# Kernel tuning notes

Hardware: AMD Instinct MI355X
Metric: run time of the kernel (lower is better)

The kernel has to match this reference:

```python
import jax, jax.numpy as jnp
import numpy as np

B, SQ, SK = 32, 512, 512
Q_DIM = 512
K_DIM = 512
H = 8
HD = 64
INNER = H * HD
MAX_POS = 512
SCALE = 1.0 / np.sqrt(HD)


def setup_inputs() -> dict:
    key = jax.random.key(0)
    ks = jax.random.split(key, 10)
    query = jax.random.normal(ks[0], (B, SQ, Q_DIM), dtype=jnp.float32)
    key_t = jax.random.normal(ks[1], (B, SK, K_DIM), dtype=jnp.float32)
    value = jax.random.normal(ks[2], (B, SK, K_DIM), dtype=jnp.float32)
    mask = jax.random.randint(ks[3], (B, SQ, SK), 0, 2, dtype=jnp.int32)
    # learned parameters (Linear weights stored as [in, out]; to_q/k/v have no bias)
    Wq = jax.random.normal(ks[4], (Q_DIM, INNER), dtype=jnp.float32) * 0.02
    Wk = jax.random.normal(ks[5], (K_DIM, INNER), dtype=jnp.float32) * 0.02
    Wv = jax.random.normal(ks[6], (K_DIM, INNER), dtype=jnp.float32) * 0.02
    Wo = jax.random.normal(ks[7], (INNER, Q_DIM), dtype=jnp.float32) * 0.02
    bo = jnp.zeros((Q_DIM,), dtype=jnp.float32)
    rel_pos_emb = jax.random.normal(ks[8], (MAX_POS, MAX_POS), dtype=jnp.float32) * 0.02
    return {"query": query, "key": key_t, "value": value, "mask": mask,
            "Wq": Wq, "Wk": Wk, "Wv": Wv, "Wo": Wo, "bo": bo,
            "rel_pos_emb": rel_pos_emb}


def reference(query, key, value, mask, Wq, Wk, Wv, Wo, bo, rel_pos_emb):
    # Projections (no bias for q/k/v)
    q = query @ Wq   # [B, SQ, INNER]
    k = key @ Wk     # [B, SK, INNER]
    v = value @ Wv   # [B, SK, INNER]
    # split heads -> [B, H, S, HD]
    q = q.reshape(B, SQ, H, HD).transpose(0, 2, 1, 3)
    k = k.reshape(B, SK, H, HD).transpose(0, 2, 1, 3)
    v = v.reshape(B, SK, H, HD).transpose(0, 2, 1, 3)
    # scaled scores + learned relative-position bias (shared across batch/heads)
    scores = jnp.einsum('bhqd,bhkd->bhqk', q, k) * SCALE
    bias = rel_pos_emb[:SQ, :SK]          # [SQ, SK]
    scores = scores + bias[None, None, :, :]
    # additive masking: positions where mask == 0 get -inf
    scores = jnp.where(mask[:, None, :, :] == 0, -jnp.inf, scores)
    attn = jax.nn.softmax(scores, axis=-1)
    # dropout is identity in eval mode (p treated as inference)
    out = jnp.einsum('bhqk,bhkd->bhqd', attn, v)
    out = out.transpose(0, 2, 1, 3).reshape(B, SQ, INNER)
    return out @ Wo + bo
```

## Files before the change

kernel.cpp:

```cpp
#include <hip/hip_runtime.h>
#include <stdint.h>


typedef unsigned short u16;
typedef __attribute__((ext_vector_type(4))) float f32x4;
typedef __attribute__((ext_vector_type(8))) __bf16 bf16x8;
typedef __attribute__((ext_vector_type(4))) unsigned short u16x4;
typedef __attribute__((ext_vector_type(8))) unsigned short u16x8;
typedef __attribute__((ext_vector_type(4))) int i32x4;
typedef __attribute__((ext_vector_type(4))) _Float16 f16x4;
typedef __attribute__((ext_vector_type(8))) _Float16 f16x8;

#define MFMA16(a, b, c) __builtin_amdgcn_mfma_f32_16x16x32_bf16((a), (b), (c), 0, 0, 0)

__device__ __forceinline__ u16 f2bf(float f) {
  unsigned u = __float_as_uint(f);
  u += 0x7fffu + ((u >> 16) & 1u);
  return (u16)(u >> 16);
}
__device__ __forceinline__ float bf2f(u16 h) {
  return __uint_as_float(((unsigned)h) << 16);
}

__device__ __forceinline__ void gl_lds16(const void* g, void* l) {
  __builtin_amdgcn_global_load_lds(
      (const __attribute__((address_space(1))) unsigned int*)g,
      (__attribute__((address_space(3))) unsigned int*)l, 16, 0, 0);
}

__global__ __launch_bounds__(256) void k_prep(
    const float* __restrict__ Wq, const float* __restrict__ Wk,
    const float* __restrict__ Wv, const float* __restrict__ Wo,
    u16* __restrict__ Wt, u16* __restrict__ WoHi, u16* __restrict__ WoLo) {
  int idx = blockIdx.x * 256 + threadIdx.x;
  int n = idx >> 9, k = idx & 511;
  int src = k * 512 + n;
  Wt[idx]          = f2bf(Wq[src]);
  Wt[262144 + idx] = f2bf(Wk[src]);
  Wt[524288 + idx] = f2bf(Wv[src]);
  float wo = Wo[src];
  u16 hi = f2bf(wo);
  WoHi[idx] = hi;
  WoLo[idx] = f2bf(wo - bf2f(hi));
}

__global__ __launch_bounds__(256) void k_mb(
    const int* __restrict__ mask, const float* __restrict__ bias,
    _Float16* __restrict__ MB) {
  size_t i8 = ((size_t)blockIdx.x * 256 + threadIdx.x) * 8;
  i32x4 m0 = *(const i32x4*)&mask[i8];
  i32x4 m1 = *(const i32x4*)&mask[i8 + 4];
  size_t bi = i8 & 262143;
  f32x4 b0 = *(const f32x4*)&bias[bi];
  f32x4 b1 = *(const f32x4*)&bias[bi + 4];
  const _Float16 MASKED = (_Float16)(-60000.0f);
  f16x8 o;
#pragma unroll
  for (int e = 0; e < 4; ++e) {
    o[e]     = (m0[e] != 0) ? (_Float16)b0[e] : MASKED;
    o[e + 4] = (m1[e] != 0) ? (_Float16)b1[e] : MASKED;
  }
  *(f16x8*)&MB[i8] = o;
}

__global__ __launch_bounds__(512) void k_proj(
    const float* __restrict__ Xq, const float* __restrict__ Xk, const float* __restrict__ Xv,
    const u16* __restrict__ Wt,
    u16* __restrict__ Qb, u16* __restrict__ Kb, u16* __restrict__ Vtb) {
  __shared__ u16 lA[128][40];
  __shared__ u16 lB[256][40];
  const int mat = blockIdx.z;
  const float* __restrict__ A = (mat == 0) ? Xq : (mat == 1) ? Xk : Xv;
  const u16* __restrict__ Bw = Wt + (size_t)mat * 262144;
  const int tid = threadIdx.x;
  const int lane = tid & 63, wid = tid >> 6;
  const int wm = wid >> 2, wn = wid & 3;
  const int m0 = blockIdx.y * 128, n0 = blockIdx.x * 256;
  const int fr = lane & 15, g = lane >> 4;
  const int arow = tid >> 3, acg = tid & 7;
  f32x4 acc[4][4] = {};

  for (int kt = 0; kt < 16; ++kt) {
    const int k0 = kt * 32;
#pragma unroll
    for (int p = 0; p < 2; ++p) {
      int row = p * 64 + arow;
      f32x4 v = *(const f32x4*)&A[(size_t)(m0 + row) * 512 + k0 + acg * 4];
      u16x4 hv;
      hv[0] = f2bf(v[0]); hv[1] = f2bf(v[1]); hv[2] = f2bf(v[2]); hv[3] = f2bf(v[3]);
      *(u16x4*)&lA[row][acg * 4] = hv;
    }
#pragma unroll
    for (int p = 0; p < 2; ++p) {
      int idx = p * 512 + tid;
      int row = idx >> 2, cg = idx & 3;
      *(u16x8*)&lB[row][cg * 8] = *(const u16x8*)&Bw[(size_t)(n0 + row) * 512 + k0 + cg * 8];
    }
    __syncthreads();
    bf16x8 af[4], bfr[4];
#pragma unroll
    for (int fm = 0; fm < 4; ++fm)
      af[fm] = *(const bf16x8*)&lA[wm * 64 + fm * 16 + fr][g * 8];
#pragma unroll
    for (int fn = 0; fn < 4; ++fn)
      bfr[fn] = *(const bf16x8*)&lB[wn * 64 + fn * 16 + fr][g * 8];
#pragma unroll
    for (int fm = 0; fm < 4; ++fm)
#pragma unroll
      for (int fn = 0; fn < 4; ++fn)
        acc[fm][fn] = MFMA16(af[fm], bfr[fn], acc[fm][fn]);
    __syncthreads();
  }

  if (mat < 2) {
    u16* __restrict__ Out = (mat == 0) ? Qb : Kb;
#pragma unroll
    for (int fm = 0; fm < 4; ++fm) {
#pragma unroll
      for (int fn = 0; fn < 4; ++fn) {
        int gn = n0 + wn * 64 + fn * 16 + fr;
        int hh = gn >> 6, hd = gn & 63;
#pragma unroll
        for (int r = 0; r < 4; ++r) {
          int gm = m0 + wm * 64 + fm * 16 + g * 4 + r;
          int b = gm >> 9, sq = gm & 511;
          Out[(size_t)((b * 8 + hh) * 512 + sq) * 64 + hd] = f2bf(acc[fm][fn][r]);
        }
      }
    }
  } else {
#pragma unroll
    for (int fm = 0; fm < 4; ++fm) {
      int gm0 = m0 + wm * 64 + fm * 16 + g * 4;
      int b = gm0 >> 9, sq0 = gm0 & 511;
#pragma unroll
      for (int fn = 0; fn < 4; ++fn) {
        int gn = n0 + wn * 64 + fn * 16 + fr;
        int hh = gn >> 6, hd = gn & 63;
        u16x4 pv;
        pv[0] = f2bf(acc[fm][fn][0]); pv[1] = f2bf(acc[fm][fn][1]);
        pv[2] = f2bf(acc[fm][fn][2]); pv[3] = f2bf(acc[fm][fn][3]);
        *(u16x4*)&Vtb[(size_t)((b * 8 + hh) * 64 + hd) * 512 + sq0] = pv;
      }
    }
  }
}

__global__ __launch_bounds__(256, 4) void k_attn(
    const u16* __restrict__ Qb, const u16* __restrict__ Kb, const u16* __restrict__ Vtb,
    const _Float16* __restrict__ MB, float* __restrict__ Obuf) {
  __shared__ __align__(16) u16 kbuf[2][64][64];
  __shared__ __align__(16) u16 vbuf[2][64][64];
  __shared__ __align__(16) u16 lP[4][16][64];
  const int tid = threadIdx.x, lane = tid & 63, w = tid >> 6;
  const int orig = blockIdx.x;
  const int xcd = orig & 7, idx = orig >> 3;
  const int qq = idx & 3, h = (idx >> 2) & 7;
  const int b = xcd + 8 * (idx >> 5);
  const int bh = b * 8 + h;
  const int fr = lane & 15, g = lane >> 4;
  const int sq0 = qq * 128 + w * 32;
  const int sw = (fr & 7) << 4;
  const u16* __restrict__ Qh = Qb + (size_t)bh * 32768;
  const u16* __restrict__ Kh = Kb + (size_t)bh * 32768;
  const u16* __restrict__ Vh = Vtb + (size_t)bh * 32768;
  const _Float16* __restrict__ MBr = MB + (size_t)b * 262144 + (size_t)(sq0 + fr) * 512;
  char* lProw = (char*)&lP[w][fr][0];
  const char* kcb;
  const char* vcb;

  const int sub = lane >> 3;
  const int xo = ((lane & 7) ^ sub) * 8;

  bf16x8 qf[2][2];
#pragma unroll
  for (int qfi = 0; qfi < 2; ++qfi)
#pragma unroll
    for (int kc = 0; kc < 2; ++kc)
      qf[qfi][kc] = *(const bf16x8*)&Qh[(size_t)(sq0 + qfi * 16 + fr) * 64 + kc * 32 + g * 8];

  f32x4 oacc[2][4] = {};
  float mrow[2] = {-1e30f, -1e30f}, lrow[2] = {0.f, 0.f};

  {
    if (w < 2) {
      const int rb = w * 32;
      const u16* gs = Kh + (size_t)(rb + sub) * 64 + xo;
#pragma unroll
      for (int i = 0; i < 4; ++i)
        gl_lds16(gs + (size_t)i * 8 * 64, &kbuf[0][rb + i * 8][0]);
    } else {
      const int rb = (w - 2) * 32;
      const u16* gs = Vh + (size_t)(rb + sub) * 512 + xo;
#pragma unroll
      for (int i = 0; i < 4; ++i)
        gl_lds16(gs + (size_t)i * 8 * 512, &vbuf[0][rb + i * 8][0]);
    }
  }
  __syncthreads();

  int cur = 0;
  for (int kt = 0; kt < 8; ++kt) {
    const int sk0 = kt * 64;
    f16x4 mbv[2][4];
#pragma unroll
    for (int qfi = 0; qfi < 2; ++qfi)
#pragma unroll
      for (int fn = 0; fn < 4; ++fn)
        mbv[qfi][fn] = *(const f16x4*)&MBr[(size_t)qfi * 16 * 512 + sk0 + fn * 16 + g * 4];
    if (kt < 7) {
      const int nb = cur ^ 1, sk0n = sk0 + 64;
      if (w < 2) {
        const int rb = w * 32;
        const u16* gs = Kh + (size_t)(sk0n + rb + sub) * 64 + xo;
#pragma unroll
        for (int i = 0; i < 4; ++i)
          gl_lds16(gs + (size_t)i * 8 * 64, &kbuf[nb][rb + i * 8][0]);
      } else {
        const int rb = (w - 2) * 32;
        const u16* gs = Vh + (size_t)(rb + sub) * 512 + sk0n + xo;
#pragma unroll
        for (int i = 0; i < 4; ++i)
          gl_lds16(gs + (size_t)i * 8 * 512, &vbuf[nb][rb + i * 8][0]);
      }
    }
    kcb = (const char*)kbuf[cur];
    vcb = (const char*)vbuf[cur];
    f32x4 sacc[2][4] = {};
#pragma unroll
    for (int fn = 0; fn < 4; ++fn) {
      const int r = fn * 16 + fr;
      bf16x8 kf0 = *(const bf16x8*)(kcb + (size_t)r * 128 + ((0 * 64 + g * 16) ^ sw));
      bf16x8 kf1 = *(const bf16x8*)(kcb + (size_t)r * 128 + ((1 * 64 + g * 16) ^ sw));
      sacc[0][fn] = MFMA16(kf0, qf[0][0], sacc[0][fn]);
      sacc[0][fn] = MFMA16(kf1, qf[0][1], sacc[0][fn]);
      sacc[1][fn] = MFMA16(kf0, qf[1][0], sacc[1][fn]);
      sacc[1][fn] = MFMA16(kf1, qf[1][1], sacc[1][fn]);
    }
#pragma unroll
    for (int qfi = 0; qfi < 2; ++qfi)
#pragma unroll
      for (int fn = 0; fn < 4; ++fn)
#pragma unroll
        for (int r = 0; r < 4; ++r)
          sacc[qfi][fn][r] = sacc[qfi][fn][r] * 0.125f + (float)mbv[qfi][fn][r];

#pragma unroll
    for (int qfi = 0; qfi < 2; ++qfi) {
      float t0 = fmaxf(fmaxf(sacc[qfi][0][0], sacc[qfi][0][1]),
                       fmaxf(sacc[qfi][0][2], sacc[qfi][0][3]));
      float t1 = fmaxf(fmaxf(sacc[qfi][1][0], sacc[qfi][1][1]),
                       fmaxf(sacc[qfi][1][2], sacc[qfi][1][3]));
      float t2 = fmaxf(fmaxf(sacc[qfi][2][0], sacc[qfi][2][1]),
                       fmaxf(sacc[qfi][2][2], sacc[qfi][2][3]));
      float t3 = fmaxf(fmaxf(sacc[qfi][3][0], sacc[qfi][3][1]),
                       fmaxf(sacc[qfi][3][2], sacc[qfi][3][3]));
      float pm = fmaxf(fmaxf(t0, t1), fmaxf(t2, t3));
      pm = fmaxf(pm, __shfl_xor(pm, 16));
      pm = fmaxf(pm, __shfl_xor(pm, 32));
      if (!__all(pm - mrow[qfi] <= 8.0f)) {
        float mn = fmaxf(mrow[qfi], pm);
        float sfac = __expf(mrow[qfi] - mn);
        mrow[qfi] = mn;
        lrow[qfi] *= sfac;
#pragma unroll
        for (int r = 0; r < 4; ++r) {
          float sr = __shfl(sfac, g * 4 + r);
#pragma unroll
          for (int fnh = 0; fnh < 4; ++fnh)
            oacc[qfi][fnh][r] *= sr;
        }
      }
      float ps = 0.f;
#pragma unroll
      for (int fn = 0; fn < 4; ++fn) {
        float p0 = __expf(sacc[qfi][fn][0] - mrow[qfi]);
        float p1 = __expf(sacc[qfi][fn][1] - mrow[qfi]);
        float p2 = __expf(sacc[qfi][fn][2] - mrow[qfi]);
        float p3 = __expf(sacc[qfi][fn][3] - mrow[qfi]);
        ps += (p0 + p1) + (p2 + p3);
        u16x4 pw;
        pw[0] = f2bf(p0); pw[1] = f2bf(p1); pw[2] = f2bf(p2); pw[3] = f2bf(p3);
        *(u16x4*)(lProw + ((fn * 32 + g * 8) ^ sw)) = pw;
      }
      ps += __shfl_xor(ps, 16);
      ps += __shfl_xor(ps, 32);
      lrow[qfi] += ps;
      __builtin_amdgcn_wave_barrier();
#pragma unroll
      for (int kc = 0; kc < 2; ++kc) {
        bf16x8 pf = *(const bf16x8*)(lProw + ((kc * 64 + g * 16) ^ sw));
#pragma unroll
        for (int fnh = 0; fnh < 4; ++fnh) {
          const int vr = fnh * 16 + fr;
          bf16x8 vf = *(const bf16x8*)(vcb + (size_t)vr * 128 + ((kc * 64 + g * 16) ^ sw));
          oacc[qfi][fnh] = MFMA16(pf, vf, oacc[qfi][fnh]);
        }
      }
      __builtin_amdgcn_wave_barrier();
    }
    __syncthreads();
    cur ^= 1;
  }
#pragma unroll
  for (int qfi = 0; qfi < 2; ++qfi) {
#pragma unroll
    for (int r = 0; r < 4; ++r) {
      float lr = __shfl(lrow[qfi], g * 4 + r);
      float inv = 1.0f / lr;
      const int sq = sq0 + qfi * 16 + g * 4 + r;
      float* orow = &Obuf[((size_t)b * 512 + sq) * 512 + h * 64];
#pragma unroll
      for (int fnh = 0; fnh < 4; ++fnh)
        orow[fnh * 16 + fr] = oacc[qfi][fnh][r] * inv;
    }
  }
}

__global__ __launch_bounds__(512) void k_out(
    const float* __restrict__ Oin, const u16* __restrict__ WoHi, const u16* __restrict__ WoLo,
    const float* __restrict__ bo, float* __restrict__ out) {
  __shared__ u16 lAh[128][40], lAl[128][40];
  __shared__ u16 lBh[256][40], lBl[256][40];
  const int tid = threadIdx.x;
  const int lane = tid & 63, wid = tid >> 6;
  const int wm = wid >> 2, wn = wid & 3;
  const int m0 = blockIdx.y * 128, n0 = blockIdx.x * 256;
  const int fr = lane & 15, g = lane >> 4;
  const int arow = tid >> 3, acg = tid & 7;
  f32x4 acc[4][4] = {};

  for (int kt = 0; kt < 16; ++kt) {
    const int k0 = kt * 32;
#pragma unroll
    for (int p = 0; p < 2; ++p) {
      int row = p * 64 + arow;
      f32x4 v = *(const f32x4*)&Oin[(size_t)(m0 + row) * 512 + k0 + acg * 4];
      u16x4 hv, lv;
#pragma unroll
      for (int e = 0; e < 4; ++e) {
        u16 hb = f2bf(v[e]);
        hv[e] = hb;
        lv[e] = f2bf(v[e] - bf2f(hb));
      }
      *(u16x4*)&lAh[row][acg * 4] = hv;
      *(u16x4*)&lAl[row][acg * 4] = lv;
    }
#pragma unroll
    for (int p = 0; p < 2; ++p) {
      int idx = p * 512 + tid;
      int row = idx >> 2, cg = idx & 3;
      *(u16x8*)&lBh[row][cg * 8] = *(const u16x8*)&WoHi[(size_t)(n0 + row) * 512 + k0 + cg * 8];
      *(u16x8*)&lBl[row][cg * 8] = *(const u16x8*)&WoLo[(size_t)(n0 + row) * 512 + k0 + cg * 8];
    }
    __syncthreads();
    bf16x8 ah[4], al[4];
#pragma unroll
    for (int fm = 0; fm < 4; ++fm) {
      ah[fm] = *(const bf16x8*)&lAh[wm * 64 + fm * 16 + fr][g * 8];
      al[fm] = *(const bf16x8*)&lAl[wm * 64 + fm * 16 + fr][g * 8];
    }
#pragma unroll
    for (int fn = 0; fn < 4; ++fn) {
      bf16x8 bh = *(const bf16x8*)&lBh[wn * 64 + fn * 16 + fr][g * 8];
      bf16x8 bl = *(const bf16x8*)&lBl[wn * 64 + fn * 16 + fr][g * 8];
#pragma unroll
      for (int fm = 0; fm < 4; ++fm) {
        acc[fm][fn] = MFMA16(ah[fm], bh, acc[fm][fn]);
        acc[fm][fn] = MFMA16(ah[fm], bl, acc[fm][fn]);
        acc[fm][fn] = MFMA16(al[fm], bh, acc[fm][fn]);
      }
    }
    __syncthreads();
  }
#pragma unroll
  for (int fm = 0; fm < 4; ++fm) {
#pragma unroll
    for (int fn = 0; fn < 4; ++fn) {
      int gn = n0 + wn * 64 + fn * 16 + fr;
      float bv = bo[gn];
#pragma unroll
      for (int r = 0; r < 4; ++r) {
        int gm = m0 + wm * 64 + fm * 16 + g * 4 + r;
        out[(size_t)gm * 512 + gn] = acc[fm][fn][r] + bv;
      }
    }
  }
}

extern "C" void kernel_launch(void* const* d_in, const int* in_sizes, int n_in,
                              void* d_out, int out_size, void* d_ws, size_t ws_size,
                              hipStream_t stream) {
  (void)in_sizes; (void)n_in; (void)out_size; (void)ws_size;
  const float* query = (const float*)d_in[0];
  const float* key_t = (const float*)d_in[1];
  const float* value = (const float*)d_in[2];
  const int*   mask  = (const int*)d_in[3];
  const float* Wq    = (const float*)d_in[4];
  const float* Wk    = (const float*)d_in[5];
  const float* Wv    = (const float*)d_in[6];
  const float* Wo    = (const float*)d_in[7];
  const float* bo    = (const float*)d_in[8];
  const float* bias  = (const float*)d_in[9];
  float* out = (float*)d_out;

  char* p = (char*)d_ws;
  u16* Wt   = (u16*)p; p += (size_t)3 * 512 * 512 * 2;
  u16* WoHi = (u16*)p; p += (size_t)512 * 512 * 2;
  u16* WoLo = (u16*)p; p += (size_t)512 * 512 * 2;
  u16* Qb   = (u16*)p; p += (size_t)32 * 8 * 512 * 64 * 2;
  u16* Kb   = (u16*)p; p += (size_t)32 * 8 * 512 * 64 * 2;
  u16* Vtb  = (u16*)p; p += (size_t)32 * 8 * 512 * 64 * 2;
  float* Obuf = (float*)p; p += (size_t)32 * 512 * 512 * 4;
  _Float16* MBp = (_Float16*)p;

  k_prep<<<1024, 256, 0, stream>>>(Wq, Wk, Wv, Wo, Wt, WoHi, WoLo);
  k_mb<<<4096, 256, 0, stream>>>(mask, bias, MBp);
  k_proj<<<dim3(2, 128, 3), 512, 0, stream>>>(query, key_t, value, Wt, Qb, Kb, Vtb);
  k_attn<<<1024, 256, 0, stream>>>(Qb, Kb, Vtb, MBp, Obuf);
  k_out<<<dim3(2, 128), 512, 0, stream>>>(Obuf, WoHi, WoLo, bo, out);
}
```

Measured before the change: 185.4 us.

## Restructure projection and output GEMMs with direct-register weight loads and double-buffered A tiles

```diff
diff --git a/kernel.cpp b/kernel.cpp
--- a/kernel.cpp
+++ b/kernel.cpp
@@ -12,6 +12,13 @@
 typedef __attribute__((ext_vector_type(8))) _Float16 f16x8;
 
 #define MFMA16(a, b, c) __builtin_amdgcn_mfma_f32_16x16x32_bf16((a), (b), (c), 0, 0, 0)
+
+#define LGKM0_BARRIER()                                        \
+  do {                                                         \
+    asm volatile("s_waitcnt lgkmcnt(0)" ::: "memory");         \
+    __builtin_amdgcn_s_barrier();                              \
+    __builtin_amdgcn_sched_barrier(0);                         \
+  } while (0)
 
 __device__ __forceinline__ u16 f2bf(float f) {
   unsigned u = __float_as_uint(f);
@@ -63,53 +70,68 @@
   *(f16x8*)&MB[i8] = o;
 }
 
-__global__ __launch_bounds__(512) void k_proj(
+__global__ __launch_bounds__(256, 4) void k_proj(
     const float* __restrict__ Xq, const float* __restrict__ Xk, const float* __restrict__ Xv,
     const u16* __restrict__ Wt,
     u16* __restrict__ Qb, u16* __restrict__ Kb, u16* __restrict__ Vtb) {
-  __shared__ u16 lA[128][40];
-  __shared__ u16 lB[256][40];
+  __shared__ __align__(16) u16 lA[2][64][40];
   const int mat = blockIdx.z;
   const float* __restrict__ A = (mat == 0) ? Xq : (mat == 1) ? Xk : Xv;
   const u16* __restrict__ Bw = Wt + (size_t)mat * 262144;
-  const int tid = threadIdx.x;
-  const int lane = tid & 63, wid = tid >> 6;
-  const int wm = wid >> 2, wn = wid & 3;
-  const int m0 = blockIdx.y * 128, n0 = blockIdx.x * 256;
+  const int tid = threadIdx.x, lane = tid & 63, wn = tid >> 6;
+  const int m0 = blockIdx.y * 64, n0 = blockIdx.x * 256;
   const int fr = lane & 15, g = lane >> 4;
-  const int arow = tid >> 3, acg = tid & 7;
+  const int arow = tid >> 2, acg = tid & 3;
+  const float* __restrict__ Ar = &A[(size_t)(m0 + arow) * 512 + acg * 8];
+  const u16* __restrict__ Bp[4];
+#pragma unroll
+  for (int fn = 0; fn < 4; ++fn)
+    Bp[fn] = &Bw[(size_t)(n0 + wn * 64 + fn * 16 + fr) * 512 + g * 8];
+
   f32x4 acc[4][4] = {};
-
+  f32x4 va[2][2];
+  bf16x8 bB[4];
+
+  {
+    f32x4 v0 = *(const f32x4*)&Ar[0];
+    f32x4 v1 = *(const f32x4*)&Ar[4];
+    va[0][0] = *(const f32x4*)&Ar[32];
+    va[0][1] = *(const f32x4*)&Ar[36];
+    u16x8 hv;
+#pragma unroll
+    for (int e = 0; e < 4; ++e) { hv[e] = f2bf(v0[e]); hv[e + 4] = f2bf(v1[e]); }
+    *(u16x8*)&lA[0][arow][acg * 8] = hv;
+  }
+  LGKM0_BARRIER();
+
+#pragma unroll
   for (int kt = 0; kt < 16; ++kt) {
+    const int cur = kt & 1, nxt = cur ^ 1;
     const int k0 = kt * 32;
 #pragma unroll
-    for (int p = 0; p < 2; ++p) {
-      int row = p * 64 + arow;
-      f32x4 v = *(const f32x4*)&A[(size_t)(m0 + row) * 512 + k0 + acg * 4];
-      u16x4 hv;
-      hv[0] = f2bf(v[0]); hv[1] = f2bf(v[1]); hv[2] = f2bf(v[2]); hv[3] = f2bf(v[3]);
-      *(u16x4*)&lA[row][acg * 4] = hv;
-    }
-#pragma unroll
-    for (int p = 0; p < 2; ++p) {
-      int idx = p * 512 + tid;
-      int row = idx >> 2, cg = idx & 3;
-      *(u16x8*)&lB[row][cg * 8] = *(const u16x8*)&Bw[(size_t)(n0 + row) * 512 + k0 + cg * 8];
-    }
-    __syncthreads();
-    bf16x8 af[4], bfr[4];
-#pragma unroll
-    for (int fm = 0; fm < 4; ++fm)
-      af[fm] = *(const bf16x8*)&lA[wm * 64 + fm * 16 + fr][g * 8];
-#pragma unroll
     for (int fn = 0; fn < 4; ++fn)
-      bfr[fn] = *(const bf16x8*)&lB[wn * 64 + fn * 16 + fr][g * 8];
-#pragma unroll
-    for (int fm = 0; fm < 4; ++fm)
+      bB[fn] = *(const bf16x8*)(Bp[fn] + k0);
+    if (kt < 14) {
+      va[nxt][0] = *(const f32x4*)&Ar[(kt + 2) * 32];
+      va[nxt][1] = *(const f32x4*)&Ar[(kt + 2) * 32 + 4];
+    }
+#pragma unroll
+    for (int fm = 0; fm < 4; ++fm) {
+      bf16x8 af = *(const bf16x8*)&lA[cur][fm * 16 + fr][g * 8];
 #pragma unroll
       for (int fn = 0; fn < 4; ++fn)
-        acc[fm][fn] = MFMA16(af[fm], bfr[fn], acc[fm][fn]);
-    __syncthreads();
+        acc[fm][fn] = MFMA16(af, bB[fn], acc[fm][fn]);
+    }
+    if (kt < 15) {
+      u16x8 hv;
+#pragma unroll
+      for (int e = 0; e < 4; ++e) {
+        hv[e]     = f2bf(va[cur][0][e]);
+        hv[e + 4] = f2bf(va[cur][1][e]);
+      }
+      *(u16x8*)&lA[nxt][arow][acg * 8] = hv;
+    }
+    LGKM0_BARRIER();
   }
 
   if (mat < 2) {
@@ -122,7 +144,7 @@
         int hh = gn >> 6, hd = gn & 63;
 #pragma unroll
         for (int r = 0; r < 4; ++r) {
-          int gm = m0 + wm * 64 + fm * 16 + g * 4 + r;
+          int gm = m0 + fm * 16 + g * 4 + r;
           int b = gm >> 9, sq = gm & 511;
           Out[(size_t)((b * 8 + hh) * 512 + sq) * 64 + hd] = f2bf(acc[fm][fn][r]);
         }
@@ -131,7 +153,7 @@
   } else {
 #pragma unroll
     for (int fm = 0; fm < 4; ++fm) {
-      int gm0 = m0 + wm * 64 + fm * 16 + g * 4;
+      int gm0 = m0 + fm * 16 + g * 4;
       int b = gm0 >> 9, sq0 = gm0 & 511;
 #pragma unroll
       for (int fn = 0; fn < 4; ++fn) {
@@ -317,71 +339,88 @@
   }
 }
 
-__global__ __launch_bounds__(512) void k_out(
+__global__ __launch_bounds__(512, 4) void k_out(
     const float* __restrict__ Oin, const u16* __restrict__ WoHi, const u16* __restrict__ WoLo,
     const float* __restrict__ bo, float* __restrict__ out) {
-  __shared__ u16 lAh[128][40], lAl[128][40];
-  __shared__ u16 lBh[256][40], lBl[256][40];
-  const int tid = threadIdx.x;
-  const int lane = tid & 63, wid = tid >> 6;
-  const int wm = wid >> 2, wn = wid & 3;
-  const int m0 = blockIdx.y * 128, n0 = blockIdx.x * 256;
+  __shared__ __align__(16) u16 lAh[2][64][40], lAl[2][64][40];
+  const int tid = threadIdx.x, lane = tid & 63, wn = tid >> 6;
+  const int m0 = blockIdx.y * 64, n0 = blockIdx.x * 256;
   const int fr = lane & 15, g = lane >> 4;
   const int arow = tid >> 3, acg = tid & 7;
-  f32x4 acc[4][4] = {};
-
+  const float* __restrict__ Ar = &Oin[(size_t)(m0 + arow) * 512 + acg * 4];
+  const u16* __restrict__ Bh[2];
+  const u16* __restrict__ Bl[2];
+#pragma unroll
+  for (int fn = 0; fn < 2; ++fn) {
+    size_t row = (size_t)(n0 + wn * 32 + fn * 16 + fr) * 512 + g * 8;
+    Bh[fn] = &WoHi[row];
+    Bl[fn] = &WoLo[row];
+  }
+
+  f32x4 acc[4][2] = {};
+  f32x4 va[2];
+
+  {
+    f32x4 v = *(const f32x4*)&Ar[0];
+    va[0] = *(const f32x4*)&Ar[32];
+    u16x4 hv, lv;
+#pragma unroll
+    for (int e = 0; e < 4; ++e) {
+      u16 hb = f2bf(v[e]);
+      hv[e] = hb;
+      lv[e] = f2bf(v[e] - bf2f(hb));
+    }
+    *(u16x4*)&lAh[0][arow][acg * 4] = hv;
+    *(u16x4*)&lAl[0][arow][acg * 4] = lv;
+  }
+  LGKM0_BARRIER();
+
+#pragma unroll
   for (int kt = 0; kt < 16; ++kt) {
+    const int cur = kt & 1, nxt = cur ^ 1;
     const int k0 = kt * 32;
-#pragma unroll
-    for (int p = 0; p < 2; ++p) {
-      int row = p * 64 + arow;
-      f32x4 v = *(const f32x4*)&Oin[(size_t)(m0 + row) * 512 + k0 + acg * 4];
+    bf16x8 bh[2], bl[2];
+#pragma unroll
+    for (int fn = 0; fn < 2; ++fn) {
+      bh[fn] = *(const bf16x8*)(Bh[fn] + k0);
+      bl[fn] = *(const bf16x8*)(Bl[fn] + k0);
+    }
+    if (kt < 14)
+      va[nxt] = *(const f32x4*)&Ar[(kt + 2) * 32];
+#pragma unroll
+    for (int fm = 0; fm < 4; ++fm) {
+      bf16x8 ah = *(const bf16x8*)&lAh[cur][fm * 16 + fr][g * 8];
+      bf16x8 al = *(const bf16x8*)&lAl[cur][fm * 16 + fr][g * 8];
+#pragma unroll
+      for (int fn = 0; fn < 2; ++fn) {
+        acc[fm][fn] = MFMA16(ah, bh[fn], acc[fm][fn]);
+        acc[fm][fn] = MFMA16(ah, bl[fn], acc[fm][fn]);
+        acc[fm][fn] = MFMA16(al, bh[fn], acc[fm][fn]);
+      }
+    }
+    if (kt < 15) {
       u16x4 hv, lv;
 #pragma unroll
       for (int e = 0; e < 4; ++e) {
-        u16 hb = f2bf(v[e]);
+        u16 hb = f2bf(va[cur][e]);
         hv[e] = hb;
-        lv[e] = f2bf(v[e] - bf2f(hb));
-      }
-      *(u16x4*)&lAh[row][acg * 4] = hv;
-      *(u16x4*)&lAl[row][acg * 4] = lv;
-    }
-#pragma unroll
-    for (int p = 0; p < 2; ++p) {
-      int idx = p * 512 + tid;
-      int row = idx >> 2, cg = idx & 3;
-      *(u16x8*)&lBh[row][cg * 8] = *(const u16x8*)&WoHi[(size_t)(n0 + row) * 512 + k0 + cg * 8];
-      *(u16x8*)&lBl[row][cg * 8] = *(const u16x8*)&WoLo[(size_t)(n0 + row) * 512 + k0 + cg * 8];
-    }
-    __syncthreads();
-    bf16x8 ah[4], al[4];
-#pragma unroll
-    for (int fm = 0; fm < 4; ++fm) {
-      ah[fm] = *(const bf16x8*)&lAh[wm * 64 + fm * 16 + fr][g * 8];
-      al[fm] = *(const bf16x8*)&lAl[wm * 64 + fm * 16 + fr][g * 8];
-    }
-#pragma unroll
-    for (int fn = 0; fn < 4; ++fn) {
-      bf16x8 bh = *(const bf16x8*)&lBh[wn * 64 + fn * 16 + fr][g * 8];
-      bf16x8 bl = *(const bf16x8*)&lBl[wn * 64 + fn * 16 + fr][g * 8];
-#pragma unroll
-      for (int fm = 0; fm < 4; ++fm) {
-        acc[fm][fn] = MFMA16(ah[fm], bh, acc[fm][fn]);
-        acc[fm][fn] = MFMA16(ah[fm], bl, acc[fm][fn]);
-        acc[fm][fn] = MFMA16(al[fm], bh, acc[fm][fn]);
-      }
-    }
-    __syncthreads();
-  }
+        lv[e] = f2bf(va[cur][e] - bf2f(hb));
+      }
+      *(u16x4*)&lAh[nxt][arow][acg * 4] = hv;
+      *(u16x4*)&lAl[nxt][arow][acg * 4] = lv;
+    }
+    LGKM0_BARRIER();
+  }
+
 #pragma unroll
   for (int fm = 0; fm < 4; ++fm) {
 #pragma unroll
-    for (int fn = 0; fn < 4; ++fn) {
-      int gn = n0 + wn * 64 + fn * 16 + fr;
+    for (int fn = 0; fn < 2; ++fn) {
+      int gn = n0 + wn * 32 + fn * 16 + fr;
       float bv = bo[gn];
 #pragma unroll
       for (int r = 0; r < 4; ++r) {
-        int gm = m0 + wm * 64 + fm * 16 + g * 4 + r;
+        int gm = m0 + fm * 16 + g * 4 + r;
         out[(size_t)gm * 512 + gn] = acc[fm][fn][r] + bv;
       }
     }
@@ -416,7 +455,7 @@
 
   k_prep<<<1024, 256, 0, stream>>>(Wq, Wk, Wv, Wo, Wt, WoHi, WoLo);
   k_mb<<<4096, 256, 0, stream>>>(mask, bias, MBp);
-  k_proj<<<dim3(2, 128, 3), 512, 0, stream>>>(query, key_t, value, Wt, Qb, Kb, Vtb);
+  k_proj<<<dim3(2, 256, 3), 256, 0, stream>>>(query, key_t, value, Wt, Qb, Kb, Vtb);
   k_attn<<<1024, 256, 0, stream>>>(Qb, Kb, Vtb, MBp, Obuf);
-  k_out<<<dim3(2, 128), 512, 0, stream>>>(Obuf, WoHi, WoLo, bo, out);
-}
+  k_out<<<dim3(2, 256), 512, 0, stream>>>(Obuf, WoHi, WoLo, bo, out);
+}
```

Measured after the change: 189.8 us. 1.02x slower.
